# Kernel tuning notes

Measured on AMD Instinct MI355X. Metric: run time of the kernel, lower is better.

The kernel has to match this reference:

```python
import jax, jax.numpy as jnp
import numpy as np

H = 1024
NH = 16
DH = H // NH

def setup_inputs() -> dict:
    key = jax.random.key(0)
    ks = jax.random.split(key, 6)
    s = 1.0 / np.sqrt(H)
    x = jax.random.normal(ks[0], (4, 2048, H), dtype=jnp.float32)
    Wq = jax.random.uniform(ks[1], (H, H), jnp.float32, -s, s)
    Wk = jax.random.uniform(ks[2], (H, H), jnp.float32, -s, s)
    Wv = jax.random.uniform(ks[3], (H, H), jnp.float32, -s, s)
    Wo = jax.random.uniform(ks[4], (H, H), jnp.float32, -s, s)
    bo = jax.random.uniform(ks[5], (H,), jnp.float32, -s, s)
    return {"x": x, "Wq": Wq, "Wk": Wk, "Wv": Wv, "Wo": Wo, "bo": bo}

def reference(x, Wq, Wk, Wv, Wo, bo):
    B, T, Hd = x.shape
    # projections: torch Linear is x @ W.T
    def split_heads(y):
        return y.reshape(B, T, NH, DH).transpose(0, 2, 1, 3)  # [B, nh, T, dh]
    Q = split_heads(x @ Wq.T)
    K = split_heads(x @ Wk.T)
    V = split_heads(x @ Wv.T)
    scores = jnp.einsum('bhtd,bhsd->bhts', Q, K) / jnp.sqrt(jnp.float32(DH))
    w = jax.nn.softmax(scores, axis=-1)
    ctx = jnp.einsum('bhts,bhsd->bhtd', w, V)  # [B, nh, T, dh]
    ctx = ctx.transpose(0, 2, 1, 3).reshape(B, T, Hd)
    out = ctx @ Wo.T + bo  # [B, T, H]
    return out.mean(axis=1)  # [B, H]
```

## Files before the change

kernel.cpp:

```cpp
#include <hip/hip_runtime.h>
#include <hip/hip_bf16.h>
#include <cstdint>

#define BB   4
#define TT   2048
#define HH   1024
#define NHH  16
#define DHH  64
#define MM   (BB*TT)
#define N3   (3*HH)

typedef __attribute__((ext_vector_type(8))) short short8;
typedef __attribute__((ext_vector_type(4))) float f32x4;

#if __has_builtin(__builtin_amdgcn_exp2f)
#define EXP2F(x) __builtin_amdgcn_exp2f(x)
#else
#define EXP2F(x) exp2f(x)
#endif

#define QSCALE 0.1803368801111204f

__device__ __forceinline__ float bf2f(unsigned short u) {
    return __uint_as_float(((uint32_t)u) << 16);
}
__device__ __forceinline__ unsigned short f2bf(float f) {
    uint32_t u = __float_as_uint(f);
    return (unsigned short)((u + 0x7fffu + ((u >> 16) & 1u)) >> 16);
}
__device__ __forceinline__ void gload_lds16(const unsigned short* g, unsigned short* l) {
    __builtin_amdgcn_global_load_lds(
        (const __attribute__((address_space(1))) uint32_t*)g,
        (__attribute__((address_space(3))) uint32_t*)l, 16, 0, 0);
}

__global__ __launch_bounds__(256) void cvt_bf16(
    const float* __restrict__ src, unsigned short* __restrict__ dst, int n4)
{
    int i = blockIdx.x * 256 + threadIdx.x;
    const int stride = gridDim.x * 256;
    for (; i < n4; i += stride) {
        float4 v = ((const float4*)src)[i];
        ushort4 o;
        o.x = f2bf(v.x); o.y = f2bf(v.y); o.z = f2bf(v.z); o.w = f2bf(v.w);
        ((ushort4*)dst)[i] = o;
    }
}

__global__ __launch_bounds__(256) void cvt_w3(
    const float* __restrict__ Wq, const float* __restrict__ Wk,
    const float* __restrict__ Wv, unsigned short* __restrict__ Wb)
{
    const float* src = (blockIdx.y == 0) ? Wq : (blockIdx.y == 1 ? Wk : Wv);
    unsigned short* dst = Wb + (size_t)blockIdx.y * HH * HH;
    const int n4 = HH * HH / 4;
    int i = blockIdx.x * 256 + threadIdx.x;
    const int stride = gridDim.x * 256;
    for (; i < n4; i += stride) {
        float4 v = ((const float4*)src)[i];
        ushort4 o;
        o.x = f2bf(v.x); o.y = f2bf(v.y); o.z = f2bf(v.z); o.w = f2bf(v.w);
        ((ushort4*)dst)[i] = o;
    }
}

__global__ __launch_bounds__(256) void proj_mfma(
    const unsigned short* __restrict__ xb, const unsigned short* __restrict__ Wb,
    unsigned short* __restrict__ qp, unsigned short* __restrict__ kp,
    unsigned short* __restrict__ vp)
{
    __shared__ unsigned short As[4096];
    __shared__ unsigned short Bs[4096];
    const int m0 = blockIdx.x * 128;
    const int n0 = blockIdx.y * 128;
    const int sel = n0 >> 10;
    const unsigned short* Wbase = Wb + (size_t)sel * HH * HH;
    const int nw0 = n0 & (HH - 1);
    const int tid = threadIdx.x;
    const int wave = tid >> 6, lane = tid & 63;
    const int quad = lane >> 4, l15 = lane & 15;
    const int wm = wave >> 1, wn = wave & 1;

    f32x4 acc[4][4];
    #pragma unroll
    for (int i = 0; i < 4; ++i)
        #pragma unroll
        for (int j = 0; j < 4; ++j) acc[i][j] = (f32x4){0.f, 0.f, 0.f, 0.f};

    for (int k0 = 0; k0 < HH; k0 += 32) {
        __syncthreads();
        #pragma unroll
        for (int q = 0; q < 2; ++q) {
            const int chunk = (wave * 2 + q) * 64 + lane;
            const int kc = chunk >> 7, mrow = chunk & 127;
            gload_lds16(xb    + (size_t)(m0  + mrow) * HH + k0 + kc * 8, As + chunk * 8);
            gload_lds16(Wbase + (size_t)(nw0 + mrow) * HH + k0 + kc * 8, Bs + chunk * 8);
        }
        __syncthreads();
        short8 af[4], bf[4];
        #pragma unroll
        for (int i = 0; i < 4; ++i)
            af[i] = *(const short8*)&As[(quad * 128 + wm * 64 + i * 16 + l15) * 8];
        #pragma unroll
        for (int j = 0; j < 4; ++j)
            bf[j] = *(const short8*)&Bs[(quad * 128 + wn * 64 + j * 16 + l15) * 8];
        #pragma unroll
        for (int i = 0; i < 4; ++i)
            #pragma unroll
            for (int j = 0; j < 4; ++j)
                acc[i][j] = __builtin_amdgcn_mfma_f32_16x16x32_bf16(af[i], bf[j], acc[i][j], 0, 0, 0);
    }
    unsigned short* outp = (sel == 0) ? qp : (sel == 1 ? kp : vp);
    const float cscale = (sel == 0) ? QSCALE : 1.0f;
    #pragma unroll
    for (int i = 0; i < 4; ++i)
        #pragma unroll
        for (int j = 0; j < 4; ++j) {
            const int col = n0 + wn * 64 + j * 16 + l15;
            const int hh2 = (col >> 6) & (NHH - 1);
            const int dd  = col & (DHH - 1);
            #pragma unroll
            for (int r = 0; r < 4; ++r) {
                const int row = m0 + wm * 64 + i * 16 + quad * 4 + r;
                const int bb2 = row >> 11, tt2 = row & (TT - 1);
                outp[((size_t)(bb2 * NHH + hh2) * TT + tt2) * DHH + dd] =
                    f2bf(acc[i][j][r] * cscale);
            }
        }
}

__global__ __launch_bounds__(256) void attn_fused(
    const unsigned short* __restrict__ qp, const unsigned short* __restrict__ kp,
    float* __restrict__ a)
{
    const int t0 = blockIdx.x * 128;
    const int h = blockIdx.y, b = blockIdx.z;
    const int bh = b * NHH + h;
    const int tid = threadIdx.x;
    const int wave = tid >> 6, lane = tid & 63;
    const int quad = lane >> 4, l15 = lane & 15;
    __shared__ float red[4][128];
    __shared__ float linv[128];

    const unsigned short* q = qp + (size_t)bh * TT * DHH;
    const unsigned short* kptr =
        kp + (size_t)bh * TT * DHH + (size_t)(wave * 512 + l15) * DHH + quad * 8;

    short8 aq[8][2];
    #pragma unroll
    for (int i = 0; i < 8; ++i)
        #pragma unroll
        for (int c = 0; c < 2; ++c)
            aq[i][c] = *(const short8*)&q[(size_t)(t0 + i * 16 + l15) * DHH + quad * 8 + c * 32];

#define KLD(ss, c) (*(const short8*)(kptr + (size_t)(ss) * 16 * DHH + (c) * 32))

    float rs[8][4];
    #pragma unroll
    for (int i = 0; i < 8; ++i)
        #pragma unroll
        for (int r = 0; r < 4; ++r) rs[i][r] = 0.f;

    {
        short8 c0a = KLD(0, 0), c0b = KLD(0, 1);
        short8 c1a = KLD(1, 0), c1b = KLD(1, 1);
        for (int ss = 0; ss < 32; ++ss) {
            const short8 ba = c0a, bb = c0b;
            c0a = c1a; c0b = c1b;
            if (ss < 30) { c1a = KLD(ss + 2, 0); c1b = KLD(ss + 2, 1); }
            #pragma unroll
            for (int i = 0; i < 8; ++i) {
                f32x4 c = (f32x4){0.f, 0.f, 0.f, 0.f};
                c = __builtin_amdgcn_mfma_f32_16x16x32_bf16(aq[i][0], ba, c, 0, 0, 0);
                c = __builtin_amdgcn_mfma_f32_16x16x32_bf16(aq[i][1], bb, c, 0, 0, 0);
                #pragma unroll
                for (int r = 0; r < 4; ++r) rs[i][r] += EXP2F(c[r]);
            }
        }
    }
    #pragma unroll
    for (int off = 1; off < 16; off <<= 1)
        #pragma unroll
        for (int i = 0; i < 8; ++i)
            #pragma unroll
            for (int r = 0; r < 4; ++r) rs[i][r] += __shfl_xor(rs[i][r], off);
    if (l15 == 0)
        #pragma unroll
        for (int i = 0; i < 8; ++i)
            #pragma unroll
            for (int r = 0; r < 4; ++r) red[wave][i * 16 + quad * 4 + r] = rs[i][r];
    __syncthreads();
    if (tid < 128) {
        const float l = red[0][tid] + red[1][tid] + red[2][tid] + red[3][tid];
        linv[tid] = 1.0f / (l * (float)TT);
    }
    __syncthreads();

    float lrv[8][4];
    #pragma unroll
    for (int i = 0; i < 8; ++i)
        #pragma unroll
        for (int r = 0; r < 4; ++r) lrv[i][r] = linv[i * 16 + quad * 4 + r];

    {
        short8 c0a = KLD(0, 0), c0b = KLD(0, 1);
        short8 c1a = KLD(1, 0), c1b = KLD(1, 1);
        for (int ss = 0; ss < 32; ++ss) {
            const short8 ba = c0a, bb = c0b;
            c0a = c1a; c0b = c1b;
            if (ss < 30) { c1a = KLD(ss + 2, 0); c1b = KLD(ss + 2, 1); }
            float cs = 0.f;
            #pragma unroll
            for (int i = 0; i < 8; ++i) {
                f32x4 c = (f32x4){0.f, 0.f, 0.f, 0.f};
                c = __builtin_amdgcn_mfma_f32_16x16x32_bf16(aq[i][0], ba, c, 0, 0, 0);
                c = __builtin_amdgcn_mfma_f32_16x16x32_bf16(aq[i][1], bb, c, 0, 0, 0);
                #pragma unroll
                for (int r = 0; r < 4; ++r) cs += EXP2F(c[r]) * lrv[i][r];
            }
            cs += __shfl_xor(cs, 16);
            cs += __shfl_xor(cs, 32);
            if (lane < 16)
                atomicAdd(&a[(size_t)bh * TT + wave * 512 + ss * 16 + l15], cs);
        }
    }
#undef KLD
}

__global__ __launch_bounds__(256) void ctx_mean(
    const unsigned short* __restrict__ vp, const float* __restrict__ a,
    float* __restrict__ cm)
{
    const int h = blockIdx.x, b = blockIdx.y, sb = blockIdx.z;
    const int tid = threadIdx.x;
    const int d = tid & 63, sg = tid >> 6;
    const int bh = b * NHH + h;
    __shared__ float red[4][64];
    float part = 0.f;
    for (int s = sb * 256 + sg; s < sb * 256 + 256; s += 4) {
        const float av = a[(size_t)bh * TT + s];
        part += av * bf2f(vp[((size_t)bh * TT + s) * DHH + d]);
    }
    red[sg][d] = part;
    __syncthreads();
    if (tid < 64)
        atomicAdd(&cm[b * HH + h * DHH + tid],
                  red[0][tid] + red[1][tid] + red[2][tid] + red[3][tid]);
}

__global__ __launch_bounds__(256) void out_proj(
    const float* __restrict__ cm, const float* __restrict__ Wo,
    const float* __restrict__ bo, float* __restrict__ out)
{
    const int b = blockIdx.y;
    const int jb = blockIdx.x;
    const int tid = threadIdx.x;
    const int j = jb * 64 + (tid >> 2);
    const int kg = tid & 3;
    __shared__ float cs[HH];
    for (int k = tid; k < HH; k += 256) cs[k] = cm[b * HH + k];
    __syncthreads();
    float acc = 0.f;
    const float* wrow = &Wo[(size_t)j * HH];
    #pragma unroll 8
    for (int i = 0; i < 64; ++i) {
        const int k = kg * 256 + i * 4;
        float4 w4 = *(const float4*)&wrow[k];
        acc += w4.x * cs[k] + w4.y * cs[k+1] + w4.z * cs[k+2] + w4.w * cs[k+3];
    }
    acc += __shfl_down(acc, 2, 4);
    acc += __shfl_down(acc, 1, 4);
    if (kg == 0) out[b * HH + j] = acc + bo[j];
}

extern "C" void kernel_launch(void* const* d_in, const int* in_sizes, int n_in,
                              void* d_out, int out_size, void* d_ws, size_t ws_size,
                              hipStream_t stream) {
    const float* x  = (const float*)d_in[0];
    const float* Wq = (const float*)d_in[1];
    const float* Wk = (const float*)d_in[2];
    const float* Wv = (const float*)d_in[3];
    const float* Wo = (const float*)d_in[4];
    const float* bo = (const float*)d_in[5];
    float* out = (float*)d_out;

    char* ws = (char*)d_ws;
    unsigned short* qp = (unsigned short*)ws;  ws += (size_t)MM * HH * 2;
    unsigned short* kp = (unsigned short*)ws;  ws += (size_t)MM * HH * 2;
    unsigned short* vp = (unsigned short*)ws;  ws += (size_t)MM * HH * 2;
    unsigned short* xb = (unsigned short*)ws;  ws += (size_t)MM * HH * 2;
    unsigned short* Wb = (unsigned short*)ws;  ws += (size_t)3 * HH * HH * 2;
    float* a  = (float*)ws;                    ws += (size_t)BB * NHH * TT * 4;
    float* cm = (float*)ws;

    hipMemsetAsync(a, 0, (size_t)(BB * NHH * TT + BB * HH) * 4, stream);

    cvt_bf16<<<2048, 256, 0, stream>>>(x, xb, MM * HH / 4);
    cvt_w3  <<<dim3(512, 3), 256, 0, stream>>>(Wq, Wk, Wv, Wb);

    proj_mfma <<<dim3(64, 24),      256, 0, stream>>>(xb, Wb, qp, kp, vp);
    attn_fused<<<dim3(16, NHH, BB), 256, 0, stream>>>(qp, kp, a);
    ctx_mean  <<<dim3(NHH, BB, 8),  256, 0, stream>>>(vp, a, cm);
    out_proj  <<<dim3(16, BB),      256, 0, stream>>>(cm, Wo, bo, out);
}
```

Baseline: 321.9 us.

## Shrink attention query tile to 32 rows for more blocks and occupancy

The attention kernel now handles 32 query rows per block instead of 128, so the grid grows fourfold and per-thread register use drops, with launch bounds requesting 8 blocks per CU. The grid axes are reordered so heads vary fastest. The K loop is unrolled by two with explicit ping-pong prefetch registers. The cost is that each K tile is re-read four times as often and four times as many atomicAdds go to the column-weight buffer.

```diff
diff --git a/kernel.cpp b/kernel.cpp
--- a/kernel.cpp
+++ b/kernel.cpp
@@ -129,102 +129,127 @@
         }
 }
 
-__global__ __launch_bounds__(256) void attn_fused(
+__global__ __launch_bounds__(256, 8) void attn_fused(
     const unsigned short* __restrict__ qp, const unsigned short* __restrict__ kp,
     float* __restrict__ a)
 {
-    const int t0 = blockIdx.x * 128;
-    const int h = blockIdx.y, b = blockIdx.z;
+    const int h = blockIdx.x, b = blockIdx.z;
+    const int t0 = blockIdx.y * 32;
     const int bh = b * NHH + h;
     const int tid = threadIdx.x;
     const int wave = tid >> 6, lane = tid & 63;
     const int quad = lane >> 4, l15 = lane & 15;
-    __shared__ float red[4][128];
-    __shared__ float linv[128];
+    __shared__ float red[4][32];
+    __shared__ float linv[32];
 
     const unsigned short* q = qp + (size_t)bh * TT * DHH;
-    const unsigned short* kptr =
+    const unsigned short* kbase =
         kp + (size_t)bh * TT * DHH + (size_t)(wave * 512 + l15) * DHH + quad * 8;
 
-    short8 aq[8][2];
-    #pragma unroll
-    for (int i = 0; i < 8; ++i)
+    short8 aq[2][2];
+    #pragma unroll
+    for (int i = 0; i < 2; ++i)
         #pragma unroll
         for (int c = 0; c < 2; ++c)
             aq[i][c] = *(const short8*)&q[(size_t)(t0 + i * 16 + l15) * DHH + quad * 8 + c * 32];
 
-#define KLD(ss, c) (*(const short8*)(kptr + (size_t)(ss) * 16 * DHH + (c) * 32))
-
-    float rs[8][4];
-    #pragma unroll
-    for (int i = 0; i < 8; ++i)
+    const f32x4 zk = {0.f, 0.f, 0.f, 0.f};
+
+    float rs[2][4];
+    #pragma unroll
+    for (int i = 0; i < 2; ++i)
         #pragma unroll
         for (int r = 0; r < 4; ++r) rs[i][r] = 0.f;
 
     {
-        short8 c0a = KLD(0, 0), c0b = KLD(0, 1);
-        short8 c1a = KLD(1, 0), c1b = KLD(1, 1);
-        for (int ss = 0; ss < 32; ++ss) {
-            const short8 ba = c0a, bb = c0b;
-            c0a = c1a; c0b = c1b;
-            if (ss < 30) { c1a = KLD(ss + 2, 0); c1b = KLD(ss + 2, 1); }
-            #pragma unroll
-            for (int i = 0; i < 8; ++i) {
-                f32x4 c = (f32x4){0.f, 0.f, 0.f, 0.f};
-                c = __builtin_amdgcn_mfma_f32_16x16x32_bf16(aq[i][0], ba, c, 0, 0, 0);
-                c = __builtin_amdgcn_mfma_f32_16x16x32_bf16(aq[i][1], bb, c, 0, 0, 0);
-                #pragma unroll
-                for (int r = 0; r < 4; ++r) rs[i][r] += EXP2F(c[r]);
-            }
+        short8 A0 = *(const short8*)(kbase);
+        short8 B0 = *(const short8*)(kbase + 32);
+        short8 A1 = *(const short8*)(kbase + 1024);
+        short8 B1 = *(const short8*)(kbase + 1024 + 32);
+        const unsigned short* kw = kbase + 2048;
+        for (int ss = 0; ss < 32; ss += 2) {
+            f32x4 c0 = __builtin_amdgcn_mfma_f32_16x16x32_bf16(aq[0][0], A0, zk, 0, 0, 0);
+            c0 = __builtin_amdgcn_mfma_f32_16x16x32_bf16(aq[0][1], B0, c0, 0, 0, 0);
+            f32x4 c1 = __builtin_amdgcn_mfma_f32_16x16x32_bf16(aq[1][0], A0, zk, 0, 0, 0);
+            c1 = __builtin_amdgcn_mfma_f32_16x16x32_bf16(aq[1][1], B0, c1, 0, 0, 0);
+            A0 = *(const short8*)(kw);
+            B0 = *(const short8*)(kw + 32);
+            #pragma unroll
+            for (int r = 0; r < 4; ++r) { rs[0][r] += EXP2F(c0[r]); rs[1][r] += EXP2F(c1[r]); }
+            c0 = __builtin_amdgcn_mfma_f32_16x16x32_bf16(aq[0][0], A1, zk, 0, 0, 0);
+            c0 = __builtin_amdgcn_mfma_f32_16x16x32_bf16(aq[0][1], B1, c0, 0, 0, 0);
+            c1 = __builtin_amdgcn_mfma_f32_16x16x32_bf16(aq[1][0], A1, zk, 0, 0, 0);
+            c1 = __builtin_amdgcn_mfma_f32_16x16x32_bf16(aq[1][1], B1, c1, 0, 0, 0);
+            A1 = *(const short8*)(kw + 1024);
+            B1 = *(const short8*)(kw + 1024 + 32);
+            #pragma unroll
+            for (int r = 0; r < 4; ++r) { rs[0][r] += EXP2F(c0[r]); rs[1][r] += EXP2F(c1[r]); }
+            kw += 2048;
         }
     }
     #pragma unroll
     for (int off = 1; off < 16; off <<= 1)
         #pragma unroll
-        for (int i = 0; i < 8; ++i)
+        for (int i = 0; i < 2; ++i)
             #pragma unroll
             for (int r = 0; r < 4; ++r) rs[i][r] += __shfl_xor(rs[i][r], off);
     if (l15 == 0)
         #pragma unroll
-        for (int i = 0; i < 8; ++i)
+        for (int i = 0; i < 2; ++i)
             #pragma unroll
             for (int r = 0; r < 4; ++r) red[wave][i * 16 + quad * 4 + r] = rs[i][r];
     __syncthreads();
-    if (tid < 128) {
+    if (tid < 32) {
         const float l = red[0][tid] + red[1][tid] + red[2][tid] + red[3][tid];
         linv[tid] = 1.0f / (l * (float)TT);
     }
     __syncthreads();
 
-    float lrv[8][4];
-    #pragma unroll
-    for (int i = 0; i < 8; ++i)
+    float lrv[2][4];
+    #pragma unroll
+    for (int i = 0; i < 2; ++i)
         #pragma unroll
         for (int r = 0; r < 4; ++r) lrv[i][r] = linv[i * 16 + quad * 4 + r];
 
+    float* ap = a + (size_t)bh * TT + wave * 512 + l15;
+
     {
-        short8 c0a = KLD(0, 0), c0b = KLD(0, 1);
-        short8 c1a = KLD(1, 0), c1b = KLD(1, 1);
-        for (int ss = 0; ss < 32; ++ss) {
-            const short8 ba = c0a, bb = c0b;
-            c0a = c1a; c0b = c1b;
-            if (ss < 30) { c1a = KLD(ss + 2, 0); c1b = KLD(ss + 2, 1); }
-            float cs = 0.f;
-            #pragma unroll
-            for (int i = 0; i < 8; ++i) {
-                f32x4 c = (f32x4){0.f, 0.f, 0.f, 0.f};
-                c = __builtin_amdgcn_mfma_f32_16x16x32_bf16(aq[i][0], ba, c, 0, 0, 0);
-                c = __builtin_amdgcn_mfma_f32_16x16x32_bf16(aq[i][1], bb, c, 0, 0, 0);
-                #pragma unroll
-                for (int r = 0; r < 4; ++r) cs += EXP2F(c[r]) * lrv[i][r];
-            }
-            cs += __shfl_xor(cs, 16);
-            cs += __shfl_xor(cs, 32);
-            if (lane < 16)
-                atomicAdd(&a[(size_t)bh * TT + wave * 512 + ss * 16 + l15], cs);
+        short8 A0 = *(const short8*)(kbase);
+        short8 B0 = *(const short8*)(kbase + 32);
+        short8 A1 = *(const short8*)(kbase + 1024);
+        short8 B1 = *(const short8*)(kbase + 1024 + 32);
+        const unsigned short* kw = kbase + 2048;
+        for (int ss = 0; ss < 32; ss += 2) {
+            f32x4 c0 = __builtin_amdgcn_mfma_f32_16x16x32_bf16(aq[0][0], A0, zk, 0, 0, 0);
+            c0 = __builtin_amdgcn_mfma_f32_16x16x32_bf16(aq[0][1], B0, c0, 0, 0, 0);
+            f32x4 c1 = __builtin_amdgcn_mfma_f32_16x16x32_bf16(aq[1][0], A0, zk, 0, 0, 0);
+            c1 = __builtin_amdgcn_mfma_f32_16x16x32_bf16(aq[1][1], B0, c1, 0, 0, 0);
+            A0 = *(const short8*)(kw);
+            B0 = *(const short8*)(kw + 32);
+            float cs0 = 0.f;
+            #pragma unroll
+            for (int r = 0; r < 4; ++r)
+                cs0 += EXP2F(c0[r]) * lrv[0][r] + EXP2F(c1[r]) * lrv[1][r];
+            cs0 += __shfl_xor(cs0, 16);
+            cs0 += __shfl_xor(cs0, 32);
+            if (lane < 16) atomicAdd(&ap[ss * 16], cs0);
+
+            c0 = __builtin_amdgcn_mfma_f32_16x16x32_bf16(aq[0][0], A1, zk, 0, 0, 0);
+            c0 = __builtin_amdgcn_mfma_f32_16x16x32_bf16(aq[0][1], B1, c0, 0, 0, 0);
+            c1 = __builtin_amdgcn_mfma_f32_16x16x32_bf16(aq[1][0], A1, zk, 0, 0, 0);
+            c1 = __builtin_amdgcn_mfma_f32_16x16x32_bf16(aq[1][1], B1, c1, 0, 0, 0);
+            A1 = *(const short8*)(kw + 1024);
+            B1 = *(const short8*)(kw + 1024 + 32);
+            float cs1 = 0.f;
+            #pragma unroll
+            for (int r = 0; r < 4; ++r)
+                cs1 += EXP2F(c0[r]) * lrv[0][r] + EXP2F(c1[r]) * lrv[1][r];
+            cs1 += __shfl_xor(cs1, 16);
+            cs1 += __shfl_xor(cs1, 32);
+            if (lane < 16) atomicAdd(&ap[ss * 16 + 16], cs1);
+            kw += 2048;
         }
     }
-#undef KLD
 }
 
 __global__ __launch_bounds__(256) void ctx_mean(
@@ -299,7 +324,7 @@
     cvt_w3  <<<dim3(512, 3), 256, 0, stream>>>(Wq, Wk, Wv, Wb);
 
     proj_mfma <<<dim3(64, 24),      256, 0, stream>>>(xb, Wb, qp, kp, vp);
-    attn_fused<<<dim3(16, NHH, BB), 256, 0, stream>>>(qp, kp, a);
+    attn_fused<<<dim3(NHH, 64, BB), 256, 0, stream>>>(qp, kp, a);
     ctx_mean  <<<dim3(NHH, BB, 8),  256, 0, stream>>>(vp, a, cm);
     out_proj  <<<dim3(16, BB),      256, 0, stream>>>(cm, Wo, bo, out);
 }
```

Measured after the change: 459.2 us. +42.6%, slower.
